# Kernel tuning notes

Measured on AMD Instinct MI355X. Metric: run time of the kernel, lower is better.

The kernel has to match this reference:

```python
import jax, jax.numpy as jnp
import numpy as np

B, Q, K, H, DV = 16, 256, 256, 256, 256


def setup_inputs() -> dict:
    key = jax.random.key(0)
    ks = jax.random.split(key, 6)
    return {
        "queries": jax.random.normal(ks[0], (B, Q, H), dtype=jnp.float32),
        "keys": jax.random.normal(ks[1], (B, K, H), dtype=jnp.float32),
        "values": jax.random.normal(ks[2], (B, K, DV), dtype=jnp.float32),
        "W_q": jax.random.normal(ks[3], (H, H), dtype=jnp.float32) / np.sqrt(H),
        "W_k": jax.random.normal(ks[4], (H, H), dtype=jnp.float32) / np.sqrt(H),
        "w_v": jax.random.normal(ks[5], (H,), dtype=jnp.float32) / np.sqrt(H),
    }


def reference(queries, keys, values, W_q, W_k, w_v):
    # Linear projections (nn.Linear: x @ W.T), bias-free
    q = jnp.einsum("bqd,hd->bqh", queries, W_q)  # [B,Q,H]
    k = jnp.einsum("bkd,hd->bkh", keys, W_k)      # [B,K,H]
    # Broadcast add -> tanh -> scalar projection
    features = jnp.tanh(q[:, :, None, :] + k[:, None, :, :])  # [B,Q,K,H]
    scores = jnp.einsum("bqkh,h->bqk", features, w_v)          # [B,Q,K]
    attn = jax.nn.softmax(scores, axis=-1)                      # [B,Q,K]
    return jnp.einsum("bqk,bkv->bqv", attn, values)            # [B,Q,DV]
```

## Files before the change

kernel.cpp:

```cpp
#include <hip/hip_runtime.h>
#include <hip/hip_fp16.h>

#define Bn 16
#define Qn 256
#define Kn 256
#define Hn 256
#define DVn 256

constexpr float C2    = 2.8853900817779268f;
constexpr float LOG2E = 1.4426950408889634f;

typedef __attribute__((ext_vector_type(8))) short bf16x8;
typedef __attribute__((ext_vector_type(4))) float f32x4;

__device__ __forceinline__ float fast_exp2(float x) { return __builtin_amdgcn_exp2f(x); }
__device__ __forceinline__ float fast_rcp(float x)  { return __builtin_amdgcn_rcpf(x); }

__device__ __forceinline__ unsigned short f2bf(float x) {
    unsigned u = __float_as_uint(x);
    u += 0x7fffu + ((u >> 16) & 1u);
    return (unsigned short)(u >> 16);
}

__global__ __launch_bounds__(256)
void prep_kernel(const float* __restrict__ q, const float* __restrict__ kx,
                 const float* __restrict__ wq, const float* __restrict__ wk,
                 const float* __restrict__ V,
                 unsigned short* __restrict__ Xb, unsigned short* __restrict__ Wb,
                 float* __restrict__ Vp)
{
    const int g = blockIdx.x * 256 + threadIdx.x;
    {
        const float* xs = (g < 131072) ? (q + (size_t)g * 8)
                                       : (kx + (size_t)(g - 131072) * 8);
        float4 x0 = *(const float4*)xs;
        float4 x1 = *(const float4*)(xs + 4);
        ushort4 o0, o1;
        o0.x = f2bf(x0.x); o0.y = f2bf(x0.y); o0.z = f2bf(x0.z); o0.w = f2bf(x0.w);
        o1.x = f2bf(x1.x); o1.y = f2bf(x1.y); o1.z = f2bf(x1.z); o1.w = f2bf(x1.w);
        *(ushort4*)(Xb + (size_t)g * 8)     = o0;
        *(ushort4*)(Xb + (size_t)g * 8 + 4) = o1;
    }
    if (g < 32768) {
        const float* ws = (g < 16384) ? (wq + (size_t)g * 4)
                                      : (wk + (size_t)(g - 16384) * 4);
        float4 w0 = *(const float4*)ws;
        ushort4 o;
        o.x = f2bf(w0.x); o.y = f2bf(w0.y); o.z = f2bf(w0.z); o.w = f2bf(w0.w);
        *(ushort4*)(Wb + (size_t)g * 4) = o;
    }
    {
        const int p   = g;
        const int bk4 = p >> 8, dv = p & 255;
        const int b   = bk4 >> 6, k4 = bk4 & 63;
        const float* src = V + ((size_t)(b * Kn + 4 * k4)) * DVn + dv;
        float4 o;
        o.x = src[0 * DVn]; o.y = src[1 * DVn]; o.z = src[2 * DVn]; o.w = src[3 * DVn];
        *(float4*)(Vp + (size_t)p * 4) = o;
    }
}

__global__ __launch_bounds__(256)
void proj_mfma_kernel(const unsigned short* __restrict__ Xb,
                      const unsigned short* __restrict__ Wb,
                      float* __restrict__ Eq, unsigned short* __restrict__ Ekb)
{
    const int tid  = threadIdx.x;
    const int wvid = tid >> 6, lane = tid & 63;
    const int m0   = blockIdx.x * 16;
    const int n0   = wvid * 64;
    const bool isQ = (m0 < 4096);
    const int r16  = lane & 15, q8 = (lane >> 4) * 8;

    const unsigned short* Xrow  = Xb + (size_t)(m0 + r16) * 256 + q8;
    const unsigned short* Wbase = Wb + (isQ ? 0 : 65536);

    bf16x8 afr[8];
    #pragma unroll
    for (int s = 0; s < 8; ++s) afr[s] = *(const bf16x8*)(Xrow + s * 32);

    f32x4 acc[4];
    #pragma unroll
    for (int nt = 0; nt < 4; ++nt) {
        const unsigned short* Wrow = Wbase + (size_t)(n0 + nt * 16 + r16) * 256 + q8;
        f32x4 c = {0.f, 0.f, 0.f, 0.f};
        #pragma unroll
        for (int s = 0; s < 8; ++s) {
            bf16x8 bfr = *(const bf16x8*)(Wrow + s * 32);
            c = __builtin_amdgcn_mfma_f32_16x16x32_bf16(afr[s], bfr, c, 0, 0, 0);
        }
        acc[nt] = c;
    }
    const int rbase = (lane >> 4) * 4;
    #pragma unroll
    for (int nt = 0; nt < 4; ++nt) {
        const int n = n0 + nt * 16 + r16;
        #pragma unroll
        for (int r = 0; r < 4; ++r) {
            const int m = m0 + rbase + r;
            const float val = fast_exp2(C2 * acc[nt][r]);
            if (isQ) {
                Eq[(size_t)m * 256 + n] = val;
            } else {
                const int kr = m - 4096, b = kr >> 8, kk = kr & 255;
                Ekb[(((size_t)(b * 64 + (n >> 2))) * 256 + kk) * 4 + (n & 3)] = f2bf(val);
            }
        }
    }
}

__global__ __launch_bounds__(256)
void fused_attn_kernel(const float* __restrict__ Eq, const unsigned short* __restrict__ Ekb,
                       const float* __restrict__ wv, const float* __restrict__ Vp,
                       float* __restrict__ out)
{
    const int b  = blockIdx.y;
    const int q0 = blockIdx.x * 4;
    __shared__ __align__(16) float sPv[256 * 4];
    __shared__ float sredM[4][4];
    __shared__ float sredS[4][4];
    const int tid = threadIdx.x;

    const float* eq0 = Eq + (size_t)(b * Qn + q0) * Hn;

    float sc[4] = {0.f, 0.f, 0.f, 0.f};
    const uint2* ekp = (const uint2*)Ekb + (size_t)b * 16384 + tid;
    uint2 e[4];
    #pragma unroll
    for (int g = 0; g < 4; ++g) e[g] = ekp[g * 256];
    for (int it = 0; it < 16; ++it) {
        uint2 en[4];
        if (it < 15) {
            #pragma unroll
            for (int g = 0; g < 4; ++g) en[g] = ekp[(4 * (it + 1) + g) * 256];
        }
        const int h0 = it * 16;
        float ek[16];
        #pragma unroll
        for (int g = 0; g < 4; ++g) {
            ek[4*g+0] = __uint_as_float(e[g].x << 16);
            ek[4*g+1] = __uint_as_float(e[g].x & 0xFFFF0000u);
            ek[4*g+2] = __uint_as_float(e[g].y << 16);
            ek[4*g+3] = __uint_as_float(e[g].y & 0xFFFF0000u);
        }
        #pragma unroll
        for (int g = 0; g < 4; ++g) {
            const float4 wa = *(const float4*)(wv + h0 + 4 * g);
            #pragma unroll
            for (int qq = 0; qq < 4; ++qq) {
                const float4 ea = *(const float4*)(eq0 + qq * 256 + h0 + 4 * g);
                float a = sc[qq];
                a = fmaf(wa.x, fast_rcp(fmaf(ea.x, ek[4*g+0], 1.f)), a);
                a = fmaf(wa.y, fast_rcp(fmaf(ea.y, ek[4*g+1], 1.f)), a);
                a = fmaf(wa.z, fast_rcp(fmaf(ea.z, ek[4*g+2], 1.f)), a);
                a = fmaf(wa.w, fast_rcp(fmaf(ea.w, ek[4*g+3], 1.f)), a);
                sc[qq] = a;
            }
        }
        #pragma unroll
        for (int g = 0; g < 4; ++g) e[g] = en[g];
    }

    const int w = tid >> 6, lane = tid & 63;
    #pragma unroll
    for (int qq = 0; qq < 4; ++qq) {
        sc[qq] = -2.0f * sc[qq];
        float mx = sc[qq];
        #pragma unroll
        for (int off = 32; off; off >>= 1) mx = fmaxf(mx, __shfl_xor(mx, off, 64));
        if (lane == 0) sredM[qq][w] = mx;
    }
    __syncthreads();
    float pq[4];
    #pragma unroll
    for (int qq = 0; qq < 4; ++qq) {
        const float mx = fmaxf(fmaxf(sredM[qq][0], sredM[qq][1]),
                               fmaxf(sredM[qq][2], sredM[qq][3]));
        pq[qq] = fast_exp2(LOG2E * (sc[qq] - mx));
        float s = pq[qq];
        #pragma unroll
        for (int off = 32; off; off >>= 1) s += __shfl_xor(s, off, 64);
        if (lane == 0) sredS[qq][w] = s;
    }
    *(float4*)&sPv[tid * 4] = make_float4(pq[0], pq[1], pq[2], pq[3]);
    __syncthreads();
    float rinv[4];
    #pragma unroll
    for (int qq = 0; qq < 4; ++qq)
        rinv[qq] = fast_rcp(sredS[qq][0] + sredS[qq][1] + sredS[qq][2] + sredS[qq][3]);

    float acc[4] = {0.f, 0.f, 0.f, 0.f};
    const float4* vp = (const float4*)Vp + (size_t)b * 64 * 256 + tid;
    float4 vv = vp[0];
    for (int k4 = 0; k4 < 64; ++k4) {
        float4 vn;
        if (k4 < 63) vn = vp[(k4 + 1) * 256];
        const float vj[4] = {vv.x, vv.y, vv.z, vv.w};
        #pragma unroll
        for (int j = 0; j < 4; ++j) {
            const float4 p4 = *(const float4*)&sPv[(4 * k4 + j) * 4];
            acc[0] = fmaf(p4.x, vj[j], acc[0]);
            acc[1] = fmaf(p4.y, vj[j], acc[1]);
            acc[2] = fmaf(p4.z, vj[j], acc[2]);
            acc[3] = fmaf(p4.w, vj[j], acc[3]);
        }
        vv = vn;
    }
    float* ob = out + (size_t)(b * Qn + q0) * DVn + tid;
    ob[0 * DVn] = acc[0] * rinv[0];
    ob[1 * DVn] = acc[1] * rinv[1];
    ob[2 * DVn] = acc[2] * rinv[2];
    ob[3 * DVn] = acc[3] * rinv[3];
}

extern "C" void kernel_launch(void* const* d_in, const int* in_sizes, int n_in,
                              void* d_out, int out_size, void* d_ws, size_t ws_size,
                              hipStream_t stream) {
    const float* queries = (const float*)d_in[0];
    const float* keys    = (const float*)d_in[1];
    const float* values  = (const float*)d_in[2];
    const float* W_q     = (const float*)d_in[3];
    const float* W_k     = (const float*)d_in[4];
    const float* w_v     = (const float*)d_in[5];
    float* out = (float*)d_out;

    float*          Eq  = (float*)d_ws;
    unsigned short* Ekb = (unsigned short*)(Eq + (size_t)Bn * Qn * Hn);
    float*          Vp  = (float*)(Ekb + (size_t)Bn * Kn * Hn);
    unsigned short* Xb  = (unsigned short*)(Vp + (size_t)Bn * Kn * DVn);
    unsigned short* Wb  = Xb + (size_t)2 * Bn * Qn * Hn;

    prep_kernel<<<dim3(1024), 256, 0, stream>>>(queries, keys, W_q, W_k, values,
                                                Xb, Wb, Vp);
    proj_mfma_kernel<<<dim3(512), 256, 0, stream>>>(Xb, Wb, Eq, Ekb);
    fused_attn_kernel<<<dim3(64, 16), 256, 0, stream>>>(Eq, Ekb, w_v, Vp, out);
}
```

Baseline: 128.9 us.

## Split attention into scores kernel and fp16 MFMA P·V kernel with transposed V

The fused attention kernel is split in two. One kernel computes normalized softmax probabilities and writes them as fp16 to a workspace. A new kernel then computes P·V with 16x16x32 f16 MFMA instructions. The prep kernel now converts V to fp16 and transposes it through shared memory so it can be loaded as the MFMA operand. This swaps the scalar FMA loop over V for matrix-core work, at the cost of an extra launch, a round trip of P through global memory, and fp16 rounding of the probabilities and V.

```diff
diff --git a/kernel.cpp b/kernel.cpp
--- a/kernel.cpp
+++ b/kernel.cpp
@@ -10,8 +10,9 @@
 constexpr float C2    = 2.8853900817779268f;
 constexpr float LOG2E = 1.4426950408889634f;
 
-typedef __attribute__((ext_vector_type(8))) short bf16x8;
-typedef __attribute__((ext_vector_type(4))) float f32x4;
+typedef __attribute__((ext_vector_type(8))) short   bf16x8;
+typedef __attribute__((ext_vector_type(8))) _Float16 halfx8;
+typedef __attribute__((ext_vector_type(4))) float   f32x4;
 
 __device__ __forceinline__ float fast_exp2(float x) { return __builtin_amdgcn_exp2f(x); }
 __device__ __forceinline__ float fast_rcp(float x)  { return __builtin_amdgcn_rcpf(x); }
@@ -27,36 +28,57 @@
                  const float* __restrict__ wq, const float* __restrict__ wk,
                  const float* __restrict__ V,
                  unsigned short* __restrict__ Xb, unsigned short* __restrict__ Wb,
-                 float* __restrict__ Vp)
-{
-    const int g = blockIdx.x * 256 + threadIdx.x;
+                 _Float16* __restrict__ Vt)
+{
+    __shared__ _Float16 T[64][72];
+    const int tid = threadIdx.x;
+    const int bx  = blockIdx.x;
+    if (bx < 1024) {
+        const int g = bx * 256 + tid;
+        {
+            const float* xs = (g < 131072) ? (q + (size_t)g * 8)
+                                           : (kx + (size_t)(g - 131072) * 8);
+            float4 x0 = *(const float4*)xs;
+            float4 x1 = *(const float4*)(xs + 4);
+            ushort4 o0, o1;
+            o0.x = f2bf(x0.x); o0.y = f2bf(x0.y); o0.z = f2bf(x0.z); o0.w = f2bf(x0.w);
+            o1.x = f2bf(x1.x); o1.y = f2bf(x1.y); o1.z = f2bf(x1.z); o1.w = f2bf(x1.w);
+            *(ushort4*)(Xb + (size_t)g * 8)     = o0;
+            *(ushort4*)(Xb + (size_t)g * 8 + 4) = o1;
+        }
+        if (g < 32768) {
+            const float* ws = (g < 16384) ? (wq + (size_t)g * 4)
+                                          : (wk + (size_t)(g - 16384) * 4);
+            float4 w0 = *(const float4*)ws;
+            ushort4 o;
+            o.x = f2bf(w0.x); o.y = f2bf(w0.y); o.z = f2bf(w0.z); o.w = f2bf(w0.w);
+            *(ushort4*)(Wb + (size_t)g * 4) = o;
+        }
+        return;
+    }
+    const int tb  = bx - 1024;
+    const int b   = tb >> 4;
+    const int t2  = tb & 15;
+    const int kt  = t2 >> 2, dvt = t2 & 3;
     {
-        const float* xs = (g < 131072) ? (q + (size_t)g * 8)
-                                       : (kx + (size_t)(g - 131072) * 8);
-        float4 x0 = *(const float4*)xs;
-        float4 x1 = *(const float4*)(xs + 4);
-        ushort4 o0, o1;
-        o0.x = f2bf(x0.x); o0.y = f2bf(x0.y); o0.z = f2bf(x0.z); o0.w = f2bf(x0.w);
-        o1.x = f2bf(x1.x); o1.y = f2bf(x1.y); o1.z = f2bf(x1.z); o1.w = f2bf(x1.w);
-        *(ushort4*)(Xb + (size_t)g * 8)     = o0;
-        *(ushort4*)(Xb + (size_t)g * 8 + 4) = o1;
-    }
-    if (g < 32768) {
-        const float* ws = (g < 16384) ? (wq + (size_t)g * 4)
-                                      : (wk + (size_t)(g - 16384) * 4);
-        float4 w0 = *(const float4*)ws;
-        ushort4 o;
-        o.x = f2bf(w0.x); o.y = f2bf(w0.y); o.z = f2bf(w0.z); o.w = f2bf(w0.w);
-        *(ushort4*)(Wb + (size_t)g * 4) = o;
-    }
+        const int kk = tid >> 2, c4 = (tid & 3) * 16;
+        const float* src = V + ((size_t)(b * Kn + kt * 64 + kk)) * DVn + dvt * 64 + c4;
+        #pragma unroll
+        for (int j4 = 0; j4 < 4; ++j4) {
+            float4 v = *(const float4*)(src + j4 * 4);
+            T[c4 + j4*4 + 0][kk] = (_Float16)v.x;
+            T[c4 + j4*4 + 1][kk] = (_Float16)v.y;
+            T[c4 + j4*4 + 2][kk] = (_Float16)v.z;
+            T[c4 + j4*4 + 3][kk] = (_Float16)v.w;
+        }
+    }
+    __syncthreads();
     {
-        const int p   = g;
-        const int bk4 = p >> 8, dv = p & 255;
-        const int b   = bk4 >> 6, k4 = bk4 & 63;
-        const float* src = V + ((size_t)(b * Kn + 4 * k4)) * DVn + dv;
-        float4 o;
-        o.x = src[0 * DVn]; o.y = src[1 * DVn]; o.z = src[2 * DVn]; o.w = src[3 * DVn];
-        *(float4*)(Vp + (size_t)p * 4) = o;
+        const int d = tid >> 2, kc = (tid & 3) * 16;
+        const uint4* srcl = (const uint4*)&T[d][kc];
+        uint4* dst = (uint4*)(Vt + (size_t)b * (DVn * Kn) + (size_t)(dvt * 64 + d) * Kn + kt * 64 + kc);
+        dst[0] = srcl[0];
+        dst[1] = srcl[1];
     }
 }
 
@@ -110,13 +132,11 @@
 }
 
 __global__ __launch_bounds__(256)
-void fused_attn_kernel(const float* __restrict__ Eq, const unsigned short* __restrict__ Ekb,
-                       const float* __restrict__ wv, const float* __restrict__ Vp,
-                       float* __restrict__ out)
+void scores_kernel(const float* __restrict__ Eq, const unsigned short* __restrict__ Ekb,
+                   const float* __restrict__ wv, _Float16* __restrict__ P)
 {
     const int b  = blockIdx.y;
     const int q0 = blockIdx.x * 4;
-    __shared__ __align__(16) float sPv[256 * 4];
     __shared__ float sredM[4][4];
     __shared__ float sredS[4][4];
     const int tid = threadIdx.x;
@@ -182,35 +202,53 @@
         for (int off = 32; off; off >>= 1) s += __shfl_xor(s, off, 64);
         if (lane == 0) sredS[qq][w] = s;
     }
-    *(float4*)&sPv[tid * 4] = make_float4(pq[0], pq[1], pq[2], pq[3]);
     __syncthreads();
-    float rinv[4];
-    #pragma unroll
-    for (int qq = 0; qq < 4; ++qq)
-        rinv[qq] = fast_rcp(sredS[qq][0] + sredS[qq][1] + sredS[qq][2] + sredS[qq][3]);
-
-    float acc[4] = {0.f, 0.f, 0.f, 0.f};
-    const float4* vp = (const float4*)Vp + (size_t)b * 64 * 256 + tid;
-    float4 vv = vp[0];
-    for (int k4 = 0; k4 < 64; ++k4) {
-        float4 vn;
-        if (k4 < 63) vn = vp[(k4 + 1) * 256];
-        const float vj[4] = {vv.x, vv.y, vv.z, vv.w};
-        #pragma unroll
-        for (int j = 0; j < 4; ++j) {
-            const float4 p4 = *(const float4*)&sPv[(4 * k4 + j) * 4];
-            acc[0] = fmaf(p4.x, vj[j], acc[0]);
-            acc[1] = fmaf(p4.y, vj[j], acc[1]);
-            acc[2] = fmaf(p4.z, vj[j], acc[2]);
-            acc[3] = fmaf(p4.w, vj[j], acc[3]);
-        }
-        vv = vn;
-    }
-    float* ob = out + (size_t)(b * Qn + q0) * DVn + tid;
-    ob[0 * DVn] = acc[0] * rinv[0];
-    ob[1 * DVn] = acc[1] * rinv[1];
-    ob[2 * DVn] = acc[2] * rinv[2];
-    ob[3 * DVn] = acc[3] * rinv[3];
+    #pragma unroll
+    for (int qq = 0; qq < 4; ++qq) {
+        const float rinv = fast_rcp(sredS[qq][0] + sredS[qq][1] + sredS[qq][2] + sredS[qq][3]);
+        P[(size_t)(b * Qn + q0 + qq) * Kn + tid] = (_Float16)(pq[qq] * rinv);
+    }
+}
+
+__global__ __launch_bounds__(256)
+void pv_mfma_kernel(const _Float16* __restrict__ P, const _Float16* __restrict__ Vt,
+                    float* __restrict__ out)
+{
+    const int tid  = threadIdx.x;
+    const int wvid = tid >> 6, lane = tid & 63;
+    const int bx   = blockIdx.x;
+    const int b    = bx >> 5;
+    const int t2   = bx & 31;
+    const int q0   = (t2 >> 1) * 16;
+    const int nb   = (t2 & 1) * 128 + wvid * 32;
+    const int r16  = lane & 15, q8 = (lane >> 4) * 8;
+
+    const _Float16* Prow = P + (size_t)b * (Qn * Kn) + (size_t)(q0 + r16) * Kn + q8;
+    halfx8 afr[8];
+    #pragma unroll
+    for (int s = 0; s < 8; ++s) afr[s] = *(const halfx8*)(Prow + s * 32);
+
+    f32x4 acc[2];
+    #pragma unroll
+    for (int nt = 0; nt < 2; ++nt) {
+        const _Float16* Vrow = Vt + (size_t)b * (DVn * Kn) + (size_t)(nb + nt * 16 + r16) * Kn + q8;
+        f32x4 c = {0.f, 0.f, 0.f, 0.f};
+        #pragma unroll
+        for (int s = 0; s < 8; ++s) {
+            halfx8 bfr = *(const halfx8*)(Vrow + s * 32);
+            c = __builtin_amdgcn_mfma_f32_16x16x32_f16(afr[s], bfr, c, 0, 0, 0);
+        }
+        acc[nt] = c;
+    }
+    const int rbase = (lane >> 4) * 4;
+    #pragma unroll
+    for (int nt = 0; nt < 2; ++nt) {
+        const int n = nb + nt * 16 + r16;
+        #pragma unroll
+        for (int r = 0; r < 4; ++r) {
+            out[(size_t)(b * Qn + q0 + rbase + r) * DVn + n] = acc[nt][r];
+        }
+    }
 }
 
 extern "C" void kernel_launch(void* const* d_in, const int* in_sizes, int n_in,
@@ -224,14 +262,17 @@
     const float* w_v     = (const float*)d_in[5];
     float* out = (float*)d_out;
 
-    float*          Eq  = (float*)d_ws;
-    unsigned short* Ekb = (unsigned short*)(Eq + (size_t)Bn * Qn * Hn);
-    float*          Vp  = (float*)(Ekb + (size_t)Bn * Kn * Hn);
-    unsigned short* Xb  = (unsigned short*)(Vp + (size_t)Bn * Kn * DVn);
-    unsigned short* Wb  = Xb + (size_t)2 * Bn * Qn * Hn;
-
-    prep_kernel<<<dim3(1024), 256, 0, stream>>>(queries, keys, W_q, W_k, values,
-                                                Xb, Wb, Vp);
+    char* wsb = (char*)d_ws;
+    float*          Eq  = (float*)(wsb);
+    unsigned short* Ekb = (unsigned short*)(wsb + (4u << 20));
+    unsigned short* Xb  = (unsigned short*)(wsb + (6u << 20));
+    unsigned short* Wb  = (unsigned short*)(wsb + (10u << 20));
+    _Float16*       Vt  = (_Float16*)(wsb + (10u << 20) + (256u << 10));
+    _Float16*       P   = (_Float16*)(wsb + (12u << 20) + (256u << 10));
+
+    prep_kernel<<<dim3(1280), 256, 0, stream>>>(queries, keys, W_q, W_k, values,
+                                                Xb, Wb, Vt);
     proj_mfma_kernel<<<dim3(512), 256, 0, stream>>>(Xb, Wb, Eq, Ekb);
-    fused_attn_kernel<<<dim3(64, 16), 256, 0, stream>>>(Eq, Ekb, w_v, Vp, out);
-}
+    scores_kernel<<<dim3(64, 16), 256, 0, stream>>>(Eq, Ekb, w_v, P);
+    pv_mfma_kernel<<<dim3(512), 256, 0, stream>>>(P, Vt, out);
+}
```

New measurement: 130.3 us. Within noise of the previous version (+1.0%).
